# Performance work log

Measured on AMD Instinct MI355X. Metric: run time of the kernel, lower is better.

## Reference

```python
import jax, jax.numpy as jnp
import numpy as np

CHANNELS = 64
HIDDEN = 1024
LAYERS = 24
NODE_TYPES = 19
BN_EPS = 1e-5

N_NODES = 200000
N_EDGES = 800000
N_RULES = 50000


def setup_inputs() -> dict:
    key = jax.random.key(0)
    ks = jax.random.split(key, 16)
    nodes = jax.random.randint(ks[0], (N_NODES,), 0, NODE_TYPES)
    sources = jax.random.randint(ks[1], (N_EDGES,), 0, N_NODES)
    targets = jax.random.randint(ks[2], (N_EDGES,), 0, N_NODES)
    rules = jax.random.randint(ks[3], (N_RULES,), 0, N_NODES)
    f32 = jnp.float32
    emb = jax.random.normal(ks[4], (NODE_TYPES, CHANNELS), f32)
    # per-layer, per-direction (out/back) Conv params, stacked [LAYERS, 2, ...]
    W = jax.random.normal(ks[5], (LAYERS, 2, CHANNELS, CHANNELS), f32) * 0.125  # ~xavier
    b = jax.random.normal(ks[6], (LAYERS, 2, CHANNELS), f32) * 0.01
    gamma = 1.0 + 0.1 * jax.random.normal(ks[7], (LAYERS, 2, CHANNELS), f32)
    beta = 0.01 * jax.random.normal(ks[8], (LAYERS, 2, CHANNELS), f32)
    rmean = 0.01 * jax.random.normal(ks[9], (LAYERS, 2, CHANNELS), f32)
    rvar = jax.random.uniform(ks[10], (LAYERS, 2, CHANNELS), f32, 0.5, 1.5)
    Wh = jax.random.normal(ks[11], (HIDDEN, CHANNELS), f32) * 0.05
    bh = jax.random.normal(ks[12], (HIDDEN,), f32) * 0.01
    Wo = jax.random.normal(ks[13], (1, HIDDEN), f32) * 0.03
    return {"nodes": nodes, "sources": sources, "targets": targets, "rules": rules,
            "emb": emb, "W": W, "b": b, "gamma": gamma, "beta": beta,
            "rmean": rmean, "rvar": rvar, "Wh": Wh, "bh": bh, "Wo": Wo}


def reference(nodes, sources, targets, rules, emb, W, b, gamma, beta, rmean, rvar, Wh, bh, Wo):
    n = nodes.shape[0]

    def conv(x, src, tgt, Wi, bi, g, be, rm, rv):
        # scatter_mean of gathered source features onto target nodes
        s = jax.ops.segment_sum(x[src], tgt, num_segments=n)            # [n, C]
        cnt = jax.ops.segment_sum(jnp.ones(src.shape, x.dtype), tgt, num_segments=n)
        m = s / jnp.maximum(cnt, 1.0)[:, None]
        # eval-mode BatchNorm1d (running stats) fused as affine
        xn = (m - rm) * (g * jax.lax.rsqrt(rv + BN_EPS)) + be
        return jax.nn.relu(xn @ Wi.T + bi)

    def layer(x, p):
        Wl, bl, gl, bel, rml, rvl = p
        out = conv(x, sources, targets, Wl[0], bl[0], gl[0], bel[0], rml[0], rvl[0])
        back = conv(x, targets, sources, Wl[1], bl[1], gl[1], bel[1], rml[1], rvl[1])
        return x + out + back, None

    x = emb[nodes]                                                      # [n, C]
    x, _ = jax.lax.scan(layer, x, (W, b, gamma, beta, rmean, rvar))
    h = jax.nn.relu(x[rules] @ Wh.T + bh)                               # [R, HIDDEN]
    return (h @ Wo.T)[:, 0]                                             # [R]
```

## Files before the change

### kernel.cpp

```cpp
#include <hip/hip_runtime.h>

#define N_NODES 200000
#define N_EDGES 800000
#define N_RULES 50000
#define NLAYERS 24
#define SCAN_NB 196
#define RP_STRIDE 200064

typedef short bf16x8 __attribute__((ext_vector_type(8)));
typedef float floatx4 __attribute__((ext_vector_type(4)));

__device__ __forceinline__ unsigned short f2bf(float f) {
  unsigned int b = __float_as_uint(f);
  b += 0x7FFFu + ((b >> 16) & 1u);
  return (unsigned short)(b >> 16);
}
__device__ __forceinline__ float bf2f(unsigned short u) {
  return __uint_as_float(((unsigned int)u) << 16);
}


__global__ void k_hist(const int* __restrict__ src, const int* __restrict__ tgt,
                       int* __restrict__ deg_out, int* __restrict__ deg_back,
                       int* __restrict__ rank_out, int* __restrict__ rank_back) {
  int e = blockIdx.x * 256 + threadIdx.x;
  rank_out[e]  = atomicAdd(&deg_out[tgt[e]], 1);
  rank_back[e] = atomicAdd(&deg_back[src[e]], 1);
}

__global__ void k_scanA(const int* __restrict__ deg, int* __restrict__ part) {
  int y = blockIdx.y;
  const int* d = deg + y * N_NODES;
  __shared__ int sh[256];
  int t = threadIdx.x;
  int base = blockIdx.x * 1024 + t * 4;
  int s = 0;
  #pragma unroll
  for (int k = 0; k < 4; ++k) { int i = base + k; if (i < N_NODES) s += d[i]; }
  sh[t] = s; __syncthreads();
  for (int off = 128; off > 0; off >>= 1) { if (t < off) sh[t] += sh[t + off]; __syncthreads(); }
  if (t == 0) part[y * SCAN_NB + blockIdx.x] = sh[0];
}

__global__ void k_scanB(int* __restrict__ part, int* __restrict__ rp) {
  int y = blockIdx.y;
  __shared__ int buf[256];
  int t = threadIdx.x;
  int v = (t < SCAN_NB) ? part[y * SCAN_NB + t] : 0;
  buf[t] = v; __syncthreads();
  for (int off = 1; off < 256; off <<= 1) {
    int x = (t >= off) ? buf[t - off] : 0;
    __syncthreads();
    buf[t] += x;
    __syncthreads();
  }
  if (t < SCAN_NB) part[y * SCAN_NB + t] = buf[t] - v;
  if (t == 0) rp[y * RP_STRIDE + N_NODES] = N_EDGES;
}

__global__ void k_scanC(const int* __restrict__ deg, const int* __restrict__ part,
                        int* __restrict__ rp) {
  int y = blockIdx.y;
  const int* d = deg + y * N_NODES;
  int* r = rp + y * RP_STRIDE;
  __shared__ int buf[256];
  int t = threadIdx.x;
  int base = blockIdx.x * 1024 + t * 4;
  int dv[4]; int s = 0;
  #pragma unroll
  for (int k = 0; k < 4; ++k) { int i = base + k; dv[k] = (i < N_NODES) ? d[i] : 0; s += dv[k]; }
  buf[t] = s; __syncthreads();
  int sv = s;
  for (int off = 1; off < 256; off <<= 1) {
    int x = (t >= off) ? buf[t - off] : 0;
    __syncthreads();
    buf[t] += x;
    __syncthreads();
  }
  int e = part[y * SCAN_NB + blockIdx.x] + buf[t] - sv;
  #pragma unroll
  for (int k = 0; k < 4; ++k) { int i = base + k; if (i < N_NODES) r[i] = e; e += dv[k]; }
}

__global__ void k_fill(const int* __restrict__ src, const int* __restrict__ tgt,
                       const int* __restrict__ rp_out, const int* __restrict__ rp_back,
                       const int* __restrict__ rank_out, const int* __restrict__ rank_back,
                       int* __restrict__ ci_out, int* __restrict__ ci_back) {
  int e = blockIdx.x * 256 + threadIdx.x;
  int s = src[e], t = tgt[e];
  ci_out[rp_out[t] + rank_out[e]] = s;
  ci_back[rp_back[s] + rank_back[e]] = t;
}

__global__ void k_prep(const float* __restrict__ W, const float* __restrict__ b,
                       const float* __restrict__ gamma, const float* __restrict__ beta,
                       const float* __restrict__ rmean, const float* __restrict__ rvar,
                       unsigned short* __restrict__ WpF, float* __restrict__ bp) {
  int d = blockIdx.x, l = blockIdx.y, lane = threadIdx.x;
  int ld = l * 2 + d;
  __shared__ float s_s[64], t_s[64];
  float s = gamma[ld * 64 + lane] * rsqrtf(rvar[ld * 64 + lane] + 1e-5f);
  s_s[lane] = s;
  t_s[lane] = beta[ld * 64 + lane] - rmean[ld * 64 + lane] * s;
  __syncthreads();
  float bias = b[ld * 64 + lane];
  for (int j = 0; j < 64; ++j) bias += W[(ld * 64 + lane) * 64 + j] * t_s[j];
  bp[ld * 64 + lane] = bias;
  #pragma unroll
  for (int f = 0; f < 8; ++f) {
    int ct = f >> 1, kh = f & 1;
    int row = ct * 16 + (lane & 15);
    #pragma unroll
    for (int jj = 0; jj < 8; ++jj) {
      int k = kh * 32 + (lane >> 4) * 8 + jj;
      float val = W[(ld * 64 + row) * 64 + k] * s_s[k];
      WpF[(ld * 8 + f) * 512 + lane * 8 + jj] = f2bf(val);
    }
  }
}

__global__ void k_prep2(const float* __restrict__ Wh,
                        unsigned short* __restrict__ WhFhi,
                        unsigned short* __restrict__ WhFlo) {
  int jt = blockIdx.x, lane = threadIdx.x;
  #pragma unroll
  for (int kh = 0; kh < 2; ++kh) {
    #pragma unroll
    for (int jj = 0; jj < 8; ++jj) {
      int j = jt * 16 + (lane & 15);
      int k = kh * 32 + (lane >> 4) * 8 + jj;
      float wv = Wh[j * 64 + k];
      unsigned short hi = f2bf(wv);
      WhFhi[(jt * 2 + kh) * 512 + lane * 8 + jj] = hi;
      WhFlo[(jt * 2 + kh) * 512 + lane * 8 + jj] = f2bf(wv - bf2f(hi));
    }
  }
}

__global__ void k_embed(const int* __restrict__ nodes, const float* __restrict__ emb,
                        unsigned short* __restrict__ hi_a,
                        unsigned short* __restrict__ lo) {
  int gid = blockIdx.x * 256 + threadIdx.x;
  int i = gid >> 6, c = gid & 63;
  float v = emb[nodes[i] * 64 + c];
  unsigned short h = f2bf(v);
  hi_a[gid] = h;
  lo[gid] = f2bf(v - bf2f(h));
}

__global__ __launch_bounds__(256, 6) void k_layer(
    const unsigned short* __restrict__ hi_in,
    unsigned short* __restrict__ hi_out,
    unsigned short* __restrict__ lo,
    const int* __restrict__ rp0, const int* __restrict__ ci0,
    const int* __restrict__ rp1, const int* __restrict__ ci1,
    const unsigned short* __restrict__ WfL, const float* __restrict__ bpL) {
  __shared__ __align__(16) unsigned short m_s[4][2][16 * 72];
  __shared__ float bp_s[128];
  int tid = threadIdx.x, lane = tid & 63, w = tid >> 6;
  if (tid < 128) bp_s[tid] = bpL[tid];
  __syncthreads();
  int base = (blockIdx.x * 4 + w) * 16;
  int n15 = lane & 15, q = lane >> 4;

  int rpv0 = (lane < 17) ? rp0[base + lane] : 0;
  int rpv1 = (lane < 17) ? rp1[base + lane] : 0;
  int rs0 = __builtin_amdgcn_readlane(rpv0, 0);
  int re0 = __builtin_amdgcn_readlane(rpv0, 16);
  int rs1 = __builtin_amdgcn_readlane(rpv1, 0);
  int re1 = __builtin_amdgcn_readlane(rpv1, 16);
  int nb0 = re0 - rs0, nb1 = re1 - rs1;

  int cv0  = (lane < nb0)      ? ci0[rs0 + lane]      : 0;
  int cv1  = (lane < nb1)      ? ci1[rs1 + lane]      : 0;
  int cv0n = (64 + lane < nb0) ? ci0[rs0 + 64 + lane] : 0;
  int cv1n = (64 + lane < nb1) ? ci1[rs1 + 64 + lane] : 0;

  int cur0 = 0, cs0 = rs0, ce0 = __builtin_amdgcn_readlane(rpv0, 1);
  int cur1 = 0, cs1 = rs1, ce1 = __builtin_amdgcn_readlane(rpv1, 1);
  float a0 = 0.f, a1 = 0.f;

  int g0max = (nb0 + 15) >> 4, g1max = (nb1 + 15) >> 4;
  int gmax = g0max > g1max ? g0max : g1max;

  for (int g = 0; g < gmax; ++g) {
    int off = g << 4;
    int boff = off & 63;
    if (g && boff == 0) {
      cv0 = cv0n; cv1 = cv1n;
      cv0n = (off + 64 + lane < nb0) ? ci0[rs0 + off + 64 + lane] : 0;
      cv1n = (off + 64 + lane < nb1) ? ci1[rs1 + off + 64 + lane] : 0;
    }
    bool do0 = off < nb0, do1 = off < nb1;
    float v0[16], v1[16];
    if (do0) {
      #pragma unroll
      for (int u = 0; u < 16; ++u) {
        int sn = __builtin_amdgcn_readlane(cv0, boff + u);
        v0[u] = bf2f(hi_in[sn * 64 + lane]);
      }
    }
    if (do1) {
      #pragma unroll
      for (int u = 0; u < 16; ++u) {
        int sn = __builtin_amdgcn_readlane(cv1, boff + u);
        v1[u] = bf2f(hi_in[sn * 64 + lane]);
      }
    }
    if (do0) {
      int jb = rs0 + off;
      #pragma unroll
      for (int u = 0; u < 16; ++u) {
        int j = jb + u;
        if (j < re0) {
          while (j >= ce0) {
            int deg = ce0 - cs0;
            float invc = deg > 0 ? __builtin_amdgcn_rcpf((float)deg) : 0.f;
            m_s[w][0][cur0 * 72 + lane] = f2bf(a0 * invc);
            a0 = 0.f; cur0++; cs0 = ce0;
            ce0 = __builtin_amdgcn_readlane(rpv0, cur0 + 1);
          }
          a0 += v0[u];
        }
      }
    }
    if (do1) {
      int jb = rs1 + off;
      #pragma unroll
      for (int u = 0; u < 16; ++u) {
        int j = jb + u;
        if (j < re1) {
          while (j >= ce1) {
            int deg = ce1 - cs1;
            float invc = deg > 0 ? __builtin_amdgcn_rcpf((float)deg) : 0.f;
            m_s[w][1][cur1 * 72 + lane] = f2bf(a1 * invc);
            a1 = 0.f; cur1++; cs1 = ce1;
            ce1 = __builtin_amdgcn_readlane(rpv1, cur1 + 1);
          }
          a1 += v1[u];
        }
      }
    }
  }
  #pragma unroll 1
  while (cur0 < 16) {
    int deg = ce0 - cs0;
    float invc = deg > 0 ? __builtin_amdgcn_rcpf((float)deg) : 0.f;
    m_s[w][0][cur0 * 72 + lane] = f2bf(a0 * invc);
    a0 = 0.f; cs0 = ce0; cur0++;
    if (cur0 < 16) ce0 = __builtin_amdgcn_readlane(rpv0, cur0 + 1);
  }
  #pragma unroll 1
  while (cur1 < 16) {
    int deg = ce1 - cs1;
    float invc = deg > 0 ? __builtin_amdgcn_rcpf((float)deg) : 0.f;
    m_s[w][1][cur1 * 72 + lane] = f2bf(a1 * invc);
    a1 = 0.f; cs1 = ce1; cur1++;
    if (cur1 < 16) ce1 = __builtin_amdgcn_readlane(rpv1, cur1 + 1);
  }

  bf16x8 b0d0 = *(const bf16x8*)&m_s[w][0][n15 * 72 + q * 8];
  bf16x8 b1d0 = *(const bf16x8*)&m_s[w][0][n15 * 72 + 32 + q * 8];
  bf16x8 b0d1 = *(const bf16x8*)&m_s[w][1][n15 * 72 + q * 8];
  bf16x8 b1d1 = *(const bf16x8*)&m_s[w][1][n15 * 72 + 32 + q * 8];
  float* ys = (float*)&m_s[w][0][0];
  #pragma unroll
  for (int ct = 0; ct < 4; ++ct) {
    const unsigned short* wf0 = WfL + (ct * 2) * 512 + lane * 8;
    const unsigned short* wf1 = WfL + 4096 + (ct * 2) * 512 + lane * 8;
    floatx4 d40 = {0.f, 0.f, 0.f, 0.f};
    floatx4 d41 = {0.f, 0.f, 0.f, 0.f};
    d40 = __builtin_amdgcn_mfma_f32_16x16x32_bf16(*(const bf16x8*)wf0, b0d0, d40, 0, 0, 0);
    d40 = __builtin_amdgcn_mfma_f32_16x16x32_bf16(*(const bf16x8*)(wf0 + 512), b1d0, d40, 0, 0, 0);
    d41 = __builtin_amdgcn_mfma_f32_16x16x32_bf16(*(const bf16x8*)wf1, b0d1, d41, 0, 0, 0);
    d41 = __builtin_amdgcn_mfma_f32_16x16x32_bf16(*(const bf16x8*)(wf1 + 512), b1d1, d41, 0, 0, 0);
    int c0 = ct * 16 + q * 4;
    floatx4 yv;
    #pragma unroll
    for (int i = 0; i < 4; ++i)
      yv[i] = fmaxf(d40[i] + bp_s[c0 + i], 0.f)
            + fmaxf(d41[i] + bp_s[64 + c0 + i], 0.f);
    *(floatx4*)&ys[n15 * 68 + c0] = yv;
  }

  #pragma unroll
  for (int r = 0; r < 16; ++r) {
    int gi = (base + r) * 64 + lane;
    float xv = bf2f(hi_in[gi]) + bf2f(lo[gi]) + ys[r * 68 + lane];
    unsigned short h = f2bf(xv);
    hi_out[gi] = h;
    lo[gi] = f2bf(xv - bf2f(h));
  }
}

__global__ __launch_bounds__(256) void k_final(
    const unsigned short* __restrict__ hi, const unsigned short* __restrict__ lo,
    const int* __restrict__ rules,
    const unsigned short* __restrict__ WhFhi, const unsigned short* __restrict__ WhFlo,
    const float* __restrict__ bh, const float* __restrict__ Wo,
    float* __restrict__ out) {
  __shared__ __align__(16) float bh_s[1024], wo_s[1024];
  int tid = threadIdx.x, lane = tid & 63, w = tid >> 6;
  ((floatx4*)bh_s)[tid] = ((const floatx4*)bh)[tid];
  ((floatx4*)wo_s)[tid] = ((const floatx4*)Wo)[tid];
  __syncthreads();
  int n15 = lane & 15, q = lane >> 4;
  int rbase = (blockIdx.x * 4 + w) * 16;
  int ru = rbase + n15;
  int nd = rules[ru < N_RULES ? ru : N_RULES - 1];
  bf16x8 b0h = *(const bf16x8*)&hi[nd * 64 + q * 8];
  bf16x8 b1h = *(const bf16x8*)&hi[nd * 64 + 32 + q * 8];
  bf16x8 b0l = *(const bf16x8*)&lo[nd * 64 + q * 8];
  bf16x8 b1l = *(const bf16x8*)&lo[nd * 64 + 32 + q * 8];
  float acc = 0.f;
  #pragma unroll 4
  for (int jt = 0; jt < 64; ++jt) {
    const unsigned short* fh = WhFhi + (jt * 2) * 512 + lane * 8;
    const unsigned short* fl = WhFlo + (jt * 2) * 512 + lane * 8;
    bf16x8 a0h = *(const bf16x8*)fh;
    bf16x8 a1h = *(const bf16x8*)(fh + 512);
    bf16x8 a0l = *(const bf16x8*)fl;
    bf16x8 a1l = *(const bf16x8*)(fl + 512);
    floatx4 d4 = {0.f, 0.f, 0.f, 0.f};
    d4 = __builtin_amdgcn_mfma_f32_16x16x32_bf16(a0h, b0h, d4, 0, 0, 0);
    d4 = __builtin_amdgcn_mfma_f32_16x16x32_bf16(a1h, b1h, d4, 0, 0, 0);
    d4 = __builtin_amdgcn_mfma_f32_16x16x32_bf16(a0h, b0l, d4, 0, 0, 0);
    d4 = __builtin_amdgcn_mfma_f32_16x16x32_bf16(a1h, b1l, d4, 0, 0, 0);
    d4 = __builtin_amdgcn_mfma_f32_16x16x32_bf16(a0l, b0h, d4, 0, 0, 0);
    d4 = __builtin_amdgcn_mfma_f32_16x16x32_bf16(a1l, b1h, d4, 0, 0, 0);
    floatx4 bh4 = *(const floatx4*)&bh_s[jt * 16 + q * 4];
    floatx4 wo4 = *(const floatx4*)&wo_s[jt * 16 + q * 4];
    #pragma unroll
    for (int i = 0; i < 4; ++i)
      acc += fmaxf(d4[i] + bh4[i], 0.f) * wo4[i];
  }
  acc += __shfl_down(acc, 32);
  acc += __shfl_down(acc, 16);
  if (lane < 16 && rbase + lane < N_RULES) out[rbase + lane] = acc;
}

extern "C" void kernel_launch(void* const* d_in, const int* in_sizes, int n_in,
                              void* d_out, int out_size, void* d_ws, size_t ws_size,
                              hipStream_t stream) {
  const int* nodes = (const int*)d_in[0];
  const int* sources = (const int*)d_in[1];
  const int* targets = (const int*)d_in[2];
  const int* rules = (const int*)d_in[3];
  const float* emb = (const float*)d_in[4];
  const float* W = (const float*)d_in[5];
  const float* b = (const float*)d_in[6];
  const float* gamma = (const float*)d_in[7];
  const float* beta = (const float*)d_in[8];
  const float* rmean = (const float*)d_in[9];
  const float* rvar = (const float*)d_in[10];
  const float* Wh = (const float*)d_in[11];
  const float* bh = (const float*)d_in[12];
  const float* Wo = (const float*)d_in[13];
  float* out = (float*)d_out;

  if (ws_size < 95100000u) return;

  char* ws = (char*)d_ws;
  unsigned short* hi_a = (unsigned short*)(ws + 0);
  unsigned short* hi_b = (unsigned short*)(ws + 25600000);
  unsigned short* lo   = (unsigned short*)(ws + 51200000);
  int* deg_out  = (int*)(ws + 76800000);
  int* deg_back = (int*)(ws + 77600000);
  int* rank_out = (int*)(ws + 78400000);
  int* rank_back= (int*)(ws + 81600000);
  int* rp_out   = (int*)(ws + 84800000);
  int* rp_back  = (int*)(ws + 85600256);
  int* ci_out   = (int*)(ws + 86400512);
  int* ci_back  = (int*)(ws + 89600512);
  int* part     = (int*)(ws + 92800512);
  unsigned short* WpF   = (unsigned short*)(ws + 92802080);
  float* bp             = (float*)(ws + 93195296);
  unsigned short* WhFhi = (unsigned short*)(ws + 93207584);
  unsigned short* WhFlo = (unsigned short*)(ws + 93338656);

  (void)hipMemsetAsync(deg_out, 0, 1600000u, stream);

  k_hist<<<3125, 256, 0, stream>>>(sources, targets, deg_out, deg_back,
                                   rank_out, rank_back);
  k_scanA<<<dim3(SCAN_NB, 2), 256, 0, stream>>>(deg_out, part);
  k_scanB<<<dim3(1, 2), 256, 0, stream>>>(part, rp_out);
  k_scanC<<<dim3(SCAN_NB, 2), 256, 0, stream>>>(deg_out, part, rp_out);
  k_fill<<<3125, 256, 0, stream>>>(sources, targets, rp_out, rp_back,
                                   rank_out, rank_back, ci_out, ci_back);
  k_prep<<<dim3(2, NLAYERS), 64, 0, stream>>>(W, b, gamma, beta, rmean, rvar, WpF, bp);
  k_prep2<<<64, 64, 0, stream>>>(Wh, WhFhi, WhFlo);
  k_embed<<<50000, 256, 0, stream>>>(nodes, emb, hi_a, lo);

  const unsigned short* hin = hi_a;
  unsigned short* hout = hi_b;
  for (int l = 0; l < NLAYERS; ++l) {
    k_layer<<<3125, 256, 0, stream>>>(hin, hout, lo,
                                      rp_out, ci_out, rp_back, ci_back,
                                      WpF + (size_t)l * 8192, bp + (size_t)l * 128);
    const unsigned short* tmp = hin; hin = hout; hout = (unsigned short*)tmp;
  }
  k_final<<<782, 256, 0, stream>>>(hin, lo, rules, WhFhi, WhFlo, bh, Wo, out);
}
```

Measured before the change: 1.495 ms.

## Software-pipeline neighbor gathers with double-buffered registers in layer kernel

Restructures the gather/accumulate loop into a two-stage software pipeline: the gathers for the next 16-edge group are issued into a second register buffer before the current group is accumulated. This hides global-memory gather latency behind the segmented-sum work. Launch bounds drop from 6 to 4 waves per SIMD to make room for the doubled register arrays, which lowers occupancy and the latency hiding that comes from running more waves.

```diff
diff --git a/kernel.cpp b/kernel.cpp
--- a/kernel.cpp
+++ b/kernel.cpp
@@ -148,7 +148,7 @@
   lo[gid] = f2bf(v - bf2f(h));
 }
 
-__global__ __launch_bounds__(256, 6) void k_layer(
+__global__ __launch_bounds__(256, 4) void k_layer(
     const unsigned short* __restrict__ hi_in,
     unsigned short* __restrict__ hi_out,
     unsigned short* __restrict__ lo,
@@ -183,65 +183,83 @@
   int g0max = (nb0 + 15) >> 4, g1max = (nb1 + 15) >> 4;
   int gmax = g0max > g1max ? g0max : g1max;
 
-  for (int g = 0; g < gmax; ++g) {
-    int off = g << 4;
-    int boff = off & 63;
-    if (g && boff == 0) {
-      cv0 = cv0n; cv1 = cv1n;
-      cv0n = (off + 64 + lane < nb0) ? ci0[rs0 + off + 64 + lane] : 0;
-      cv1n = (off + 64 + lane < nb1) ? ci1[rs1 + off + 64 + lane] : 0;
-    }
-    bool do0 = off < nb0, do1 = off < nb1;
-    float v0[16], v1[16];
-    if (do0) {
-      #pragma unroll
-      for (int u = 0; u < 16; ++u) {
-        int sn = __builtin_amdgcn_readlane(cv0, boff + u);
-        v0[u] = bf2f(hi_in[sn * 64 + lane]);
-      }
-    }
-    if (do1) {
-      #pragma unroll
-      for (int u = 0; u < 16; ++u) {
-        int sn = __builtin_amdgcn_readlane(cv1, boff + u);
-        v1[u] = bf2f(hi_in[sn * 64 + lane]);
-      }
-    }
-    if (do0) {
-      int jb = rs0 + off;
-      #pragma unroll
-      for (int u = 0; u < 16; ++u) {
-        int j = jb + u;
-        if (j < re0) {
-          while (j >= ce0) {
-            int deg = ce0 - cs0;
-            float invc = deg > 0 ? __builtin_amdgcn_rcpf((float)deg) : 0.f;
-            m_s[w][0][cur0 * 72 + lane] = f2bf(a0 * invc);
-            a0 = 0.f; cur0++; cs0 = ce0;
-            ce0 = __builtin_amdgcn_readlane(rpv0, cur0 + 1);
-          }
-          a0 += v0[u];
-        }
-      }
-    }
-    if (do1) {
-      int jb = rs1 + off;
-      #pragma unroll
-      for (int u = 0; u < 16; ++u) {
-        int j = jb + u;
-        if (j < re1) {
-          while (j >= ce1) {
-            int deg = ce1 - cs1;
-            float invc = deg > 0 ? __builtin_amdgcn_rcpf((float)deg) : 0.f;
-            m_s[w][1][cur1 * 72 + lane] = f2bf(a1 * invc);
-            a1 = 0.f; cur1++; cs1 = ce1;
-            ce1 = __builtin_amdgcn_readlane(rpv1, cur1 + 1);
-          }
-          a1 += v1[u];
-        }
-      }
-    }
-  }
+#define ISSUE(V0, V1, g_)                                                 \
+  {                                                                       \
+    int off_ = (g_) << 4, boff_ = off_ & 63;                              \
+    if (off_ < nb0) {                                                     \
+      _Pragma("unroll")                                                   \
+      for (int u = 0; u < 16; ++u) {                                      \
+        int sn = __builtin_amdgcn_readlane(cv0, boff_ + u);               \
+        V0[u] = bf2f(hi_in[sn * 64 + lane]);                              \
+      }                                                                   \
+    }                                                                     \
+    if (off_ < nb1) {                                                     \
+      _Pragma("unroll")                                                   \
+      for (int u = 0; u < 16; ++u) {                                      \
+        int sn = __builtin_amdgcn_readlane(cv1, boff_ + u);               \
+        V1[u] = bf2f(hi_in[sn * 64 + lane]);                              \
+      }                                                                   \
+    }                                                                     \
+  }
+
+#define ROLL(gi_)                                                         \
+  if (((gi_) & 3) == 0) {                                                 \
+    cv0 = cv0n; cv1 = cv1n;                                               \
+    int ob_ = ((gi_) << 4) + 64;                                          \
+    cv0n = (ob_ + lane < nb0) ? ci0[rs0 + ob_ + lane] : 0;                \
+    cv1n = (ob_ + lane < nb1) ? ci1[rs1 + ob_ + lane] : 0;                \
+  }
+
+#define ACC0(V, g_)                                                       \
+  { int off_ = (g_) << 4;                                                 \
+    if (off_ < nb0) {                                                     \
+      int jb = rs0 + off_;                                                \
+      _Pragma("unroll")                                                   \
+      for (int u = 0; u < 16; ++u) {                                      \
+        int j = jb + u;                                                   \
+        if (j < re0) {                                                    \
+          while (j >= ce0) {                                              \
+            int deg = ce0 - cs0;                                          \
+            float invc = deg > 0 ? __builtin_amdgcn_rcpf((float)deg) : 0.f; \
+            m_s[w][0][cur0 * 72 + lane] = f2bf(a0 * invc);                \
+            a0 = 0.f; cur0++; cs0 = ce0;                                  \
+            ce0 = __builtin_amdgcn_readlane(rpv0, cur0 + 1);              \
+          }                                                               \
+          a0 += V[u];                                                     \
+        } } } }
+
+#define ACC1(V, g_)                                                       \
+  { int off_ = (g_) << 4;                                                 \
+    if (off_ < nb1) {                                                     \
+      int jb = rs1 + off_;                                                \
+      _Pragma("unroll")                                                   \
+      for (int u = 0; u < 16; ++u) {                                      \
+        int j = jb + u;                                                   \
+        if (j < re1) {                                                    \
+          while (j >= ce1) {                                              \
+            int deg = ce1 - cs1;                                          \
+            float invc = deg > 0 ? __builtin_amdgcn_rcpf((float)deg) : 0.f; \
+            m_s[w][1][cur1 * 72 + lane] = f2bf(a1 * invc);                \
+            a1 = 0.f; cur1++; cs1 = ce1;                                  \
+            ce1 = __builtin_amdgcn_readlane(rpv1, cur1 + 1);              \
+          }                                                               \
+          a1 += V[u];                                                     \
+        } } } }
+
+  float vA0[16], vA1[16], vB0[16], vB1[16];
+  if (gmax > 0) ISSUE(vA0, vA1, 0)
+  for (int g = 0; g < gmax; g += 2) {
+    int g1 = g + 1, g2 = g + 2;
+    if (g1 < gmax) { ROLL(g1) ISSUE(vB0, vB1, g1) }
+    ACC0(vA0, g) ACC1(vA1, g)
+    if (g2 < gmax) { ROLL(g2) ISSUE(vA0, vA1, g2) }
+    if (g1 < gmax) { ACC0(vB0, g1) ACC1(vB1, g1) }
+  }
+#undef ISSUE
+#undef ROLL
+#undef ACC0
+#undef ACC1
+
   #pragma unroll 1
   while (cur0 < 16) {
     int deg = ce0 - cs0;
```

Result: slower. 1.639 ms (+9.7%).

## Split per-wave node tiles to 8 nodes and share MFMA across wave pairs

Applied to the files above, without the earlier changes.

Each wave now gathers and averages neighbor features for 8 nodes instead of 16. Two waves pool their rows in shared memory so that one 16-node tile is formed, and each wave then runs the MFMA for only one direction (out or back). The grid doubles to 6250 blocks. The aim is to shorten the serial gather loop per wave and raise parallelism, at the cost of two block-wide barriers and extra shared memory for the fp32 outputs, which may lower occupancy.

```diff
diff --git a/kernel.cpp b/kernel.cpp
--- a/kernel.cpp
+++ b/kernel.cpp
@@ -155,20 +155,22 @@
     const int* __restrict__ rp0, const int* __restrict__ ci0,
     const int* __restrict__ rp1, const int* __restrict__ ci1,
     const unsigned short* __restrict__ WfL, const float* __restrict__ bpL) {
-  __shared__ __align__(16) unsigned short m_s[4][2][16 * 72];
+  __shared__ __align__(16) unsigned short m_s[2][2][16 * 72];
+  __shared__ __align__(16) float ys[2][2][16 * 68];
   __shared__ float bp_s[128];
   int tid = threadIdx.x, lane = tid & 63, w = tid >> 6;
   if (tid < 128) bp_s[tid] = bpL[tid];
   __syncthreads();
-  int base = (blockIdx.x * 4 + w) * 16;
+  int nbase = blockIdx.x * 32 + w * 8;
+  int t = w >> 1, rowb = (w & 1) * 8;
   int n15 = lane & 15, q = lane >> 4;
 
-  int rpv0 = (lane < 17) ? rp0[base + lane] : 0;
-  int rpv1 = (lane < 17) ? rp1[base + lane] : 0;
+  int rpv0 = (lane < 9) ? rp0[nbase + lane] : 0;
+  int rpv1 = (lane < 9) ? rp1[nbase + lane] : 0;
   int rs0 = __builtin_amdgcn_readlane(rpv0, 0);
-  int re0 = __builtin_amdgcn_readlane(rpv0, 16);
+  int re0 = __builtin_amdgcn_readlane(rpv0, 8);
   int rs1 = __builtin_amdgcn_readlane(rpv1, 0);
-  int re1 = __builtin_amdgcn_readlane(rpv1, 16);
+  int re1 = __builtin_amdgcn_readlane(rpv1, 8);
   int nb0 = re0 - rs0, nb1 = re1 - rs1;
 
   int cv0  = (lane < nb0)      ? ci0[rs0 + lane]      : 0;
@@ -216,7 +218,7 @@
           while (j >= ce0) {
             int deg = ce0 - cs0;
             float invc = deg > 0 ? __builtin_amdgcn_rcpf((float)deg) : 0.f;
-            m_s[w][0][cur0 * 72 + lane] = f2bf(a0 * invc);
+            m_s[t][0][(rowb + cur0) * 72 + lane] = f2bf(a0 * invc);
             a0 = 0.f; cur0++; cs0 = ce0;
             ce0 = __builtin_amdgcn_readlane(rpv0, cur0 + 1);
           }
@@ -233,7 +235,7 @@
           while (j >= ce1) {
             int deg = ce1 - cs1;
             float invc = deg > 0 ? __builtin_amdgcn_rcpf((float)deg) : 0.f;
-            m_s[w][1][cur1 * 72 + lane] = f2bf(a1 * invc);
+            m_s[t][1][(rowb + cur1) * 72 + lane] = f2bf(a1 * invc);
             a1 = 0.f; cur1++; cs1 = ce1;
             ce1 = __builtin_amdgcn_readlane(rpv1, cur1 + 1);
           }
@@ -243,50 +245,51 @@
     }
   }
   #pragma unroll 1
-  while (cur0 < 16) {
+  while (cur0 < 8) {
     int deg = ce0 - cs0;
     float invc = deg > 0 ? __builtin_amdgcn_rcpf((float)deg) : 0.f;
-    m_s[w][0][cur0 * 72 + lane] = f2bf(a0 * invc);
+    m_s[t][0][(rowb + cur0) * 72 + lane] = f2bf(a0 * invc);
     a0 = 0.f; cs0 = ce0; cur0++;
-    if (cur0 < 16) ce0 = __builtin_amdgcn_readlane(rpv0, cur0 + 1);
+    if (cur0 < 8) ce0 = __builtin_amdgcn_readlane(rpv0, cur0 + 1);
   }
   #pragma unroll 1
-  while (cur1 < 16) {
+  while (cur1 < 8) {
     int deg = ce1 - cs1;
     float invc = deg > 0 ? __builtin_amdgcn_rcpf((float)deg) : 0.f;
-    m_s[w][1][cur1 * 72 + lane] = f2bf(a1 * invc);
+    m_s[t][1][(rowb + cur1) * 72 + lane] = f2bf(a1 * invc);
     a1 = 0.f; cs1 = ce1; cur1++;
-    if (cur1 < 16) ce1 = __builtin_amdgcn_readlane(rpv1, cur1 + 1);
-  }
-
-  bf16x8 b0d0 = *(const bf16x8*)&m_s[w][0][n15 * 72 + q * 8];
-  bf16x8 b1d0 = *(const bf16x8*)&m_s[w][0][n15 * 72 + 32 + q * 8];
-  bf16x8 b0d1 = *(const bf16x8*)&m_s[w][1][n15 * 72 + q * 8];
-  bf16x8 b1d1 = *(const bf16x8*)&m_s[w][1][n15 * 72 + 32 + q * 8];
-  float* ys = (float*)&m_s[w][0][0];
-  #pragma unroll
-  for (int ct = 0; ct < 4; ++ct) {
-    const unsigned short* wf0 = WfL + (ct * 2) * 512 + lane * 8;
-    const unsigned short* wf1 = WfL + 4096 + (ct * 2) * 512 + lane * 8;
-    floatx4 d40 = {0.f, 0.f, 0.f, 0.f};
-    floatx4 d41 = {0.f, 0.f, 0.f, 0.f};
-    d40 = __builtin_amdgcn_mfma_f32_16x16x32_bf16(*(const bf16x8*)wf0, b0d0, d40, 0, 0, 0);
-    d40 = __builtin_amdgcn_mfma_f32_16x16x32_bf16(*(const bf16x8*)(wf0 + 512), b1d0, d40, 0, 0, 0);
-    d41 = __builtin_amdgcn_mfma_f32_16x16x32_bf16(*(const bf16x8*)wf1, b0d1, d41, 0, 0, 0);
-    d41 = __builtin_amdgcn_mfma_f32_16x16x32_bf16(*(const bf16x8*)(wf1 + 512), b1d1, d41, 0, 0, 0);
-    int c0 = ct * 16 + q * 4;
-    floatx4 yv;
+    if (cur1 < 8) ce1 = __builtin_amdgcn_readlane(rpv1, cur1 + 1);
+  }
+  __syncthreads();
+
+  {
+    int mt = w >> 1, md = w & 1;
+    bf16x8 b0 = *(const bf16x8*)&m_s[mt][md][n15 * 72 + q * 8];
+    bf16x8 b1 = *(const bf16x8*)&m_s[mt][md][n15 * 72 + 32 + q * 8];
+    const unsigned short* wf = WfL + md * 4096;
     #pragma unroll
-    for (int i = 0; i < 4; ++i)
-      yv[i] = fmaxf(d40[i] + bp_s[c0 + i], 0.f)
-            + fmaxf(d41[i] + bp_s[64 + c0 + i], 0.f);
-    *(floatx4*)&ys[n15 * 68 + c0] = yv;
-  }
-
-  #pragma unroll
-  for (int r = 0; r < 16; ++r) {
-    int gi = (base + r) * 64 + lane;
-    float xv = bf2f(hi_in[gi]) + bf2f(lo[gi]) + ys[r * 68 + lane];
+    for (int ct = 0; ct < 4; ++ct) {
+      floatx4 d4 = {0.f, 0.f, 0.f, 0.f};
+      bf16x8 a0f = *(const bf16x8*)(wf + (ct * 2 + 0) * 512 + lane * 8);
+      bf16x8 a1f = *(const bf16x8*)(wf + (ct * 2 + 1) * 512 + lane * 8);
+      d4 = __builtin_amdgcn_mfma_f32_16x16x32_bf16(a0f, b0, d4, 0, 0, 0);
+      d4 = __builtin_amdgcn_mfma_f32_16x16x32_bf16(a1f, b1, d4, 0, 0, 0);
+      int c0 = ct * 16 + q * 4;
+      floatx4 yv;
+      #pragma unroll
+      for (int i = 0; i < 4; ++i)
+        yv[i] = fmaxf(d4[i] + bp_s[md * 64 + c0 + i], 0.f);
+      *(floatx4*)&ys[mt][md][n15 * 68 + c0] = yv;
+    }
+  }
+  __syncthreads();
+
+  #pragma unroll
+  for (int r = 0; r < 8; ++r) {
+    int row = rowb + r;
+    int gi = (nbase + r) * 64 + lane;
+    float xv = bf2f(hi_in[gi]) + bf2f(lo[gi])
+             + ys[t][0][row * 68 + lane] + ys[t][1][row * 68 + lane];
     unsigned short h = f2bf(xv);
     hi_out[gi] = h;
     lo[gi] = f2bf(xv - bf2f(h));
@@ -394,7 +397,7 @@
   const unsigned short* hin = hi_a;
   unsigned short* hout = hi_b;
   for (int l = 0; l < NLAYERS; ++l) {
-    k_layer<<<3125, 256, 0, stream>>>(hin, hout, lo,
+    k_layer<<<6250, 256, 0, stream>>>(hin, hout, lo,
                                       rp_out, ci_out, rp_back, ci_back,
                                       WpF + (size_t)l * 8192, bp + (size_t)l * 128);
     const unsigned short* tmp = hin; hin = hout; hout = (unsigned short*)tmp;
```

Measured after the change: 1.687 ms. 12.9% more time.
